# Kernel tuning notes

Hardware: AMD Instinct MI355X
Metric: run time of the kernel (lower is better)

## Reference

```python
import jax, jax.numpy as jnp
import numpy as np
import math

B, T, D = 2, 2048, 2048
H, KV, Dh = 16, 4, 128
REP = H // KV
WINDOW = 1024
META = 128
ROPE_BASE = 10000.0


def _apply_rotary(x, pos):
    # x: (B, h, T, Dh), pos: (T,) -- interleaved (even/odd) RoPE as in the torch module
    dh = x.shape[-1]
    inv = 1.0 / (ROPE_BASE ** (jnp.arange(0, dh, 2, dtype=jnp.float32) / dh))  # (Dh/2,)
    freqs = pos.astype(jnp.float32)[:, None] * inv[None, :]                    # (T, Dh/2)
    cos = jnp.cos(freqs)[None, None].astype(x.dtype)
    sin = jnp.sin(freqs)[None, None].astype(x.dtype)
    x1, x2 = x[..., ::2], x[..., 1::2]
    o1 = x1 * cos - x2 * sin
    o2 = x1 * sin + x2 * cos
    return jnp.stack([o1, o2], axis=-1).reshape(x.shape)


def setup_inputs() -> dict:
    key = jax.random.key(0)
    ks = jax.random.split(key, 5)
    s = 0.02
    return {
        "x": jax.random.normal(ks[0], (B, T, D), jnp.float32),
        "Wq": jax.random.normal(ks[1], (D, H * Dh), jnp.float32) * s,
        "Wk": jax.random.normal(ks[2], (D, KV * Dh), jnp.float32) * s,
        "Wv": jax.random.normal(ks[3], (D, KV * Dh), jnp.float32) * s,
        "Wo": jax.random.normal(ks[4], (H * Dh, D), jnp.float32) * s,
    }


def reference(x, Wq, Wk, Wv, Wo):
    Bx, Tx, _ = x.shape
    # projections + head split: q (B,H,T,Dh); k,v (B,KV,T,Dh)
    q = (x @ Wq).reshape(Bx, Tx, H, Dh).transpose(0, 2, 1, 3)
    k = (x @ Wk).reshape(Bx, Tx, KV, Dh).transpose(0, 2, 1, 3)
    v = (x @ Wv).reshape(Bx, Tx, KV, Dh).transpose(0, 2, 1, 3)
    pos = jnp.arange(Tx)
    q = _apply_rotary(q, pos)
    k = _apply_rotary(k, pos)
    # GQA: repeat kv heads (expand+reshape == contiguous repeat along head axis)
    k_full = jnp.repeat(k, REP, axis=1)
    v_full = jnp.repeat(v, REP, axis=1)
    # sliding window: keep META meta tokens + last w content tokens
    w = min(WINDOW, Tx - META)
    k_full = jnp.concatenate([k_full[:, :, :META], k_full[:, :, Tx - w:]], axis=2)
    v_full = jnp.concatenate([v_full[:, :, :META], v_full[:, :, Tx - w:]], axis=2)
    Tk = META + w
    scores = jnp.einsum("bhqd,bhkd->bhqk", q, k_full) / math.sqrt(Dh)
    # torch: triu(full(-inf,(T,Tk)), diagonal=1) added to scores
    mask = jnp.arange(Tk)[None, :] > jnp.arange(Tx)[:, None]   # (T, Tk)
    scores = jnp.where(mask[None, None], -jnp.inf, scores)
    attn = jax.nn.softmax(scores, axis=-1)
    out = jnp.einsum("bhqk,bhkd->bhqd", attn, v_full)
    out = out.transpose(0, 2, 1, 3).reshape(Bx, Tx, H * Dh)
    return out @ Wo
```

## Files before the change

kernel.cpp:

```cpp
#include <hip/hip_runtime.h>
#include <hip/hip_bf16.h>
#include <math.h>

typedef __attribute__((ext_vector_type(4))) float f32x4;
typedef __attribute__((ext_vector_type(8))) short bf16x8;

#define LDSP(p)  ((__attribute__((address_space(3))) void*)(p))
#define GMEMP(p) ((const __attribute__((address_space(1))) void*)(p))

__device__ __forceinline__ short f2b(float f) {
  __hip_bfloat16 h = __float2bfloat16(f);
  return __builtin_bit_cast(short, h);
}
__device__ __forceinline__ float b2f(short s) {
  __hip_bfloat16 h = __builtin_bit_cast(__hip_bfloat16, s);
  return __bfloat162float(h);
}
__device__ __forceinline__ unsigned pack2(float a, float b) {
  return (unsigned)(unsigned short)f2b(a) | ((unsigned)(unsigned short)f2b(b) << 16);
}

__global__ void cvt_kernel(const float* __restrict__ src, short* __restrict__ dst, int n8) {
  int i = blockIdx.x * blockDim.x + threadIdx.x;
  if (i >= n8) return;
  const float4* s4 = (const float4*)src;
  float4 a = s4[2 * i], b = s4[2 * i + 1];
  bf16x8 o;
  o[0] = f2b(a.x); o[1] = f2b(a.y); o[2] = f2b(a.z); o[3] = f2b(a.w);
  o[4] = f2b(b.x); o[5] = f2b(b.y); o[6] = f2b(b.z); o[7] = f2b(b.w);
  *(bf16x8*)(dst + (size_t)i * 8) = o;
}

__global__ void transpose_kernel(const float* __restrict__ src, short* __restrict__ dst,
                                 int rows, int cols) {
  __shared__ float tile[32][33];
  int c0 = blockIdx.x * 32, r0 = blockIdx.y * 32;
  int tx = threadIdx.x & 31, ty = threadIdx.x >> 5;
  for (int i = ty; i < 32; i += 8)
    tile[i][tx] = src[(size_t)(r0 + i) * cols + c0 + tx];
  __syncthreads();
  for (int i = ty; i < 32; i += 8)
    dst[(size_t)(c0 + i) * rows + r0 + tx] = f2b(tile[tx][i]);
}

template <int OUTBF>
__global__ __launch_bounds__(256) void gemm_bt(const short* __restrict__ A,
                                               const short* __restrict__ Bt,
                                               void* __restrict__ Cv,
                                               int M, int N, int K) {
  __shared__ alignas(16) short As[128 * 32];
  __shared__ alignas(16) short Bs[128 * 32];
  const int m0 = blockIdx.y * 128, n0 = blockIdx.x * 128;
  const int wave = threadIdx.x >> 6, lane = threadIdx.x & 63;
  const int g = lane >> 4, cl = lane & 15;
  const int wr = (wave >> 1) * 64, wc = (wave & 1) * 64;
  f32x4 acc[4][4];
#pragma unroll
  for (int i = 0; i < 4; ++i)
#pragma unroll
    for (int j = 0; j < 4; ++j) acc[i][j] = (f32x4){0.f, 0.f, 0.f, 0.f};

  const size_t lda = (size_t)K;
  for (int kt = 0; kt < K; kt += 32) {
#pragma unroll
    for (int c = 0; c < 2; ++c) {
      int e = (wave * 2 + c) * 512;
      int el = e + lane * 8;
      const short* ga = A + (size_t)(m0 + (el >> 5)) * lda + kt + (el & 31);
      __builtin_amdgcn_global_load_lds(GMEMP(ga), LDSP(&As[e]), 16, 0, 0);
      const short* gb = Bt + (size_t)(n0 + (el >> 5)) * lda + kt + (el & 31);
      __builtin_amdgcn_global_load_lds(GMEMP(gb), LDSP(&Bs[e]), 16, 0, 0);
    }
    __syncthreads();
    bf16x8 af[4], bfr[4];
#pragma unroll
    for (int i = 0; i < 4; ++i)
      af[i] = *(const bf16x8*)&As[(wr + 16 * i + cl) * 32 + 8 * g];
#pragma unroll
    for (int j = 0; j < 4; ++j)
      bfr[j] = *(const bf16x8*)&Bs[(wc + 16 * j + cl) * 32 + 8 * g];
#pragma unroll
    for (int i = 0; i < 4; ++i)
#pragma unroll
      for (int j = 0; j < 4; ++j)
        acc[i][j] = __builtin_amdgcn_mfma_f32_16x16x32_bf16(af[i], bfr[j], acc[i][j], 0, 0, 0);
    __syncthreads();
  }
#pragma unroll
  for (int i = 0; i < 4; ++i)
#pragma unroll
    for (int j = 0; j < 4; ++j)
#pragma unroll
      for (int r = 0; r < 4; ++r) {
        int row = m0 + wr + 16 * i + 4 * g + r;
        int col = n0 + wc + 16 * j + cl;
        if (OUTBF)
          ((short*)Cv)[(size_t)row * N + col] = f2b(acc[i][j][r]);
        else
          ((float*)Cv)[(size_t)row * N + col] = acc[i][j][r];
      }
}

__global__ void rope_q_kernel(const short* __restrict__ qkv, short* __restrict__ qb) {
  int tid = blockIdx.x * 256 + threadIdx.x;
  int i = tid & 63;
  int h = (tid >> 6) & 15;
  int row = tid >> 10;
  int t = row & 2047;
  int b = row >> 11;
  unsigned u = *(const unsigned*)(qkv + (size_t)row * 3072 + h * 128 + 2 * i);
  float x1 = b2f((short)(u & 0xffff));
  float x2 = b2f((short)(u >> 16));
  float inv = exp2f(-0.20762050593046f * (float)i);
  float ang = (float)t * inv;
  float sn, cs;
  __sincosf(ang, &sn, &cs);
  float o1 = x1 * cs - x2 * sn;
  float o2 = x1 * sn + x2 * cs;
  unsigned w = pack2(o1, o2);
  *(unsigned*)(qb + (size_t)((b * 16 + h) * 2048 + t) * 128 + 2 * i) = w;
}

__global__ void rope_k_kernel(const short* __restrict__ qkv, short* __restrict__ ksel) {
  int tid = blockIdx.x * 256 + threadIdx.x;
  int i = tid & 63;
  int kvh = (tid >> 6) & 3;
  int row = tid >> 8;
  int t = row & 2047;
  int b = row >> 11;
  int idx = t < 128 ? t : (t >= 1024 ? t - 896 : -1);
  if (idx < 0) return;
  unsigned u = *(const unsigned*)(qkv + (size_t)row * 3072 + 2048 + kvh * 128 + 2 * i);
  float x1 = b2f((short)(u & 0xffff));
  float x2 = b2f((short)(u >> 16));
  float inv = exp2f(-0.20762050593046f * (float)i);
  float ang = (float)t * inv;
  float sn, cs;
  __sincosf(ang, &sn, &cs);
  float o1 = x1 * cs - x2 * sn;
  float o2 = x1 * sn + x2 * cs;
  unsigned w = pack2(o1, o2);
  *(unsigned*)(ksel + (size_t)((b * 4 + kvh) * 1152 + idx) * 128 + 2 * i) = w;
}

__global__ void vsel_kernel(const short* __restrict__ qkv, short* __restrict__ vt) {
  int tid = blockIdx.x * 256 + threadIdx.x;
  int idx = tid % 1152;
  int rest = tid / 1152;
  int d = rest & 127;
  int kvh = (rest >> 7) & 3;
  int b = rest >> 9;
  int t = idx < 128 ? idx : idx + 896;
  vt[(size_t)((b * 4 + kvh) * 128 + d) * 1152 + idx] =
      qkv[(size_t)(b * 2048 + t) * 3072 + 2560 + kvh * 128 + d];
}

__global__ __launch_bounds__(256) void attn_kernel(const short* __restrict__ qb,
                                                   const short* __restrict__ ksel,
                                                   const short* __restrict__ vt,
                                                   short* __restrict__ ao) {
  __shared__ alignas(16) short Ksm[2][8192];
  __shared__ alignas(16) short Vsm[8192];
  __shared__ alignas(16) short Psm[4][16][72];

  const int blk = blockIdx.x;
  const int qt = 31 - (blk >> 5);
  const int h = blk & 15, b = (blk >> 4) & 1;
  const int kv = h >> 2;
  const int wave = threadIdx.x >> 6, lane = threadIdx.x & 63;
  const int g = lane >> 4, cl = lane & 15;
  const int q0w = qt * 64 + wave * 16;
  const int qi = q0w + cl;
  const float scale = 0.08838834764831845f;
  const int niter = (qt + 1 < 18) ? (qt + 1) : 18;

  const short* kselb = ksel + (size_t)(b * 4 + kv) * 1152 * 128;
  const short* vtb = vt + (size_t)(b * 4 + kv) * 128 * 1152;

  const short* qrow = qb + (size_t)((b * 16 + h) * 2048 + qi) * 128;
  bf16x8 qf[4];
#pragma unroll
  for (int d = 0; d < 4; ++d) qf[d] = *(const bf16x8*)(qrow + d * 32 + 8 * g);

  f32x4 o[8];
#pragma unroll
  for (int c = 0; c < 8; ++c) o[c] = (f32x4){0.f, 0.f, 0.f, 0.f};
  float m_i = -1e30f, l_i = 0.f;

#pragma unroll
  for (int i = 0; i < 4; ++i) {
    int base = i * 2048 + wave * 512;
    int Lel = base + lane * 8;
    int kr = Lel >> 7;
    int kc = (Lel & 127) ^ ((kr & 7) << 3);
    __builtin_amdgcn_global_load_lds(GMEMP(kselb + (size_t)kr * 128 + kc),
                                     LDSP(&Ksm[0][base]), 16, 0, 0);
  }
  asm volatile("s_waitcnt vmcnt(0)" ::: "memory");
  __builtin_amdgcn_s_barrier();
  asm volatile("" ::: "memory");

  int cur = 0;
  for (int t = 0; t < niter; ++t) {
    const int kk0 = t * 64;
#pragma unroll
    for (int i = 0; i < 4; ++i) {
      int base = i * 2048 + wave * 512;
      int Lel = base + lane * 8;
      int vr = Lel >> 6;
      int vc = (Lel & 63) ^ ((vr & 7) << 3);
      __builtin_amdgcn_global_load_lds(GMEMP(vtb + (size_t)vr * 1152 + kk0 + vc),
                                       LDSP(&Vsm[base]), 16, 0, 0);
    }
    const bool lastk = (t + 1 >= niter);
    if (!lastk) {
#pragma unroll
      for (int i = 0; i < 4; ++i) {
        int base = i * 2048 + wave * 512;
        int Lel = base + lane * 8;
        int kr = Lel >> 7;
        int kc = (Lel & 127) ^ ((kr & 7) << 3);
        __builtin_amdgcn_global_load_lds(GMEMP(kselb + (size_t)(kk0 + 64 + kr) * 128 + kc),
                                         LDSP(&Ksm[cur ^ 1][base]), 16, 0, 0);
      }
    }

    f32x4 s[4];
#pragma unroll
    for (int j = 0; j < 4; ++j) s[j] = (f32x4){0.f, 0.f, 0.f, 0.f};
    const short* kb = &Ksm[cur][0];
    const int sw = (cl & 7) << 3;
#pragma unroll
    for (int j = 0; j < 4; ++j) {
      const int rs = (16 * j + cl) * 128;
#pragma unroll
      for (int d = 0; d < 4; ++d) {
        bf16x8 kf = *(const bf16x8*)&kb[rs + ((d * 32 + 8 * g) ^ sw)];
        s[j] = __builtin_amdgcn_mfma_f32_16x16x32_bf16(kf, qf[d], s[j], 0, 0, 0);
      }
    }

    float sv[4][4];
    float mx = -1e30f;
#pragma unroll
    for (int j = 0; j < 4; ++j)
#pragma unroll
      for (int r = 0; r < 4; ++r) {
        int key = kk0 + 16 * j + 4 * g + r;
        float v = s[j][r] * scale;
        v = (key <= qi) ? v : -1e30f;
        sv[j][r] = v;
        mx = fmaxf(mx, v);
      }
    mx = fmaxf(mx, __shfl_xor(mx, 16));
    mx = fmaxf(mx, __shfl_xor(mx, 32));
    const float mnew = fmaxf(m_i, mx);
    const float alpha = __expf(m_i - mnew);
    m_i = mnew;
    float ls = 0.f;
#pragma unroll
    for (int j = 0; j < 4; ++j) {
      float p0 = __expf(sv[j][0] - mnew);
      float p1 = __expf(sv[j][1] - mnew);
      float p2 = __expf(sv[j][2] - mnew);
      float p3 = __expf(sv[j][3] - mnew);
      ls += (p0 + p1) + (p2 + p3);
      uint2 w;
      w.x = pack2(p0, p1);
      w.y = pack2(p2, p3);
      *(uint2*)&Psm[wave][cl][16 * j + 4 * g] = w;
    }
    ls += __shfl_xor(ls, 16);
    ls += __shfl_xor(ls, 32);
    l_i = l_i * alpha + ls;
#pragma unroll
    for (int c = 0; c < 8; ++c)
#pragma unroll
      for (int r = 0; r < 4; ++r) o[c][r] *= alpha;

    if (!lastk)
      asm volatile("s_waitcnt vmcnt(4)" ::: "memory");
    else
      asm volatile("s_waitcnt vmcnt(0)" ::: "memory");
    __builtin_amdgcn_s_barrier();
    asm volatile("" ::: "memory");

    asm volatile("s_waitcnt lgkmcnt(0)" ::: "memory");
    bf16x8 pb0 = *(const bf16x8*)&Psm[wave][cl][8 * g];
    bf16x8 pb1 = *(const bf16x8*)&Psm[wave][cl][32 + 8 * g];
#pragma unroll
    for (int c = 0; c < 8; ++c) {
      const int rowd = c * 16 + cl;
      const int rvs = rowd * 64;
      bf16x8 v0 = *(const bf16x8*)&Vsm[rvs + ((8 * g) ^ sw)];
      bf16x8 v1 = *(const bf16x8*)&Vsm[rvs + ((32 + 8 * g) ^ sw)];
      o[c] = __builtin_amdgcn_mfma_f32_16x16x32_bf16(v0, pb0, o[c], 0, 0, 0);
      o[c] = __builtin_amdgcn_mfma_f32_16x16x32_bf16(v1, pb1, o[c], 0, 0, 0);
    }

    asm volatile("s_waitcnt vmcnt(0)" ::: "memory");
    __builtin_amdgcn_s_barrier();
    asm volatile("" ::: "memory");
    cur ^= 1;
  }

  short* Ol = &Ksm[0][0] + wave * 2176;
  const float invl = 1.0f / l_i;
#pragma unroll
  for (int c = 0; c < 8; ++c) {
    uint2 w;
    w.x = pack2(o[c][0] * invl, o[c][1] * invl);
    w.y = pack2(o[c][2] * invl, o[c][3] * invl);
    *(uint2*)&Ol[cl * 136 + c * 16 + 4 * g] = w;
  }
  asm volatile("s_waitcnt lgkmcnt(0)" ::: "memory");
  const int rowq = lane & 15, seg = lane >> 4;
  const short* srcl = Ol + rowq * 136 + seg * 32;
  short* dst = ao + (size_t)(b * 2048 + q0w + rowq) * 2048 + h * 128 + seg * 32;
#pragma unroll
  for (int k = 0; k < 4; ++k)
    *(bf16x8*)(dst + 8 * k) = *(const bf16x8*)(srcl + 8 * k);
}

extern "C" void kernel_launch(void* const* d_in, const int* in_sizes, int n_in,
                              void* d_out, int out_size, void* d_ws, size_t ws_size,
                              hipStream_t stream) {
  const float* x = (const float*)d_in[0];
  const float* Wq = (const float*)d_in[1];
  const float* Wk = (const float*)d_in[2];
  const float* Wv = (const float*)d_in[3];
  const float* Wo = (const float*)d_in[4];
  float* out = (float*)d_out;

  char* ws = (char*)d_ws;
  short* x_bf = (short*)ws;   ws += (size_t)4096 * 2048 * 2;
  short* wqkv_t = (short*)ws; ws += (size_t)3072 * 2048 * 2;
  short* wo_t = (short*)ws;   ws += (size_t)2048 * 2048 * 2;
  short* qkv = (short*)ws;    ws += (size_t)4096 * 3072 * 2;
  short* q_bf = (short*)ws;   ws += (size_t)2 * 16 * 2048 * 128 * 2;
  short* k_sel = (short*)ws;  ws += (size_t)2 * 4 * 1152 * 128 * 2;
  short* v_t = (short*)ws;    ws += (size_t)2 * 4 * 128 * 1152 * 2;
  short* ao = (short*)ws;     ws += (size_t)4096 * 2048 * 2;

  cvt_kernel<<<4096, 256, 0, stream>>>(x, x_bf, 1048576);
  transpose_kernel<<<dim3(64, 64), 256, 0, stream>>>(Wq, wqkv_t, 2048, 2048);
  transpose_kernel<<<dim3(16, 64), 256, 0, stream>>>(Wk, wqkv_t + (size_t)2048 * 2048, 2048, 512);
  transpose_kernel<<<dim3(16, 64), 256, 0, stream>>>(Wv, wqkv_t + (size_t)2560 * 2048, 2048, 512);
  transpose_kernel<<<dim3(64, 64), 256, 0, stream>>>(Wo, wo_t, 2048, 2048);
  gemm_bt<1><<<dim3(24, 32), 256, 0, stream>>>(x_bf, wqkv_t, qkv, 4096, 3072, 2048);
  rope_q_kernel<<<16384, 256, 0, stream>>>(qkv, q_bf);
  rope_k_kernel<<<4096, 256, 0, stream>>>(qkv, k_sel);
  vsel_kernel<<<4608, 256, 0, stream>>>(qkv, v_t);
  attn_kernel<<<1024, 256, 0, stream>>>(q_bf, k_sel, v_t, ao);
  gemm_bt<0><<<dim3(16, 32), 256, 0, stream>>>(ao, wo_t, out, 4096, 2048, 2048);
}
```

Before: 333.2 us.

## Triple-buffer GEMM with LDS swizzle, double-buffer attention V, merge small launches

The GEMM moves to a three-stage LDS pipeline with an XOR swizzle on its tiles, waits with partial vmcnt barriers, and raises wave priority around the MFMA blocks. The attention kernel double-buffers V as well as K, prefetching both for the next tile and dropping the mid-iteration barrier. The four transpose launches become one kernel, and the three RoPE/select kernels become one, to cut launch overhead. In exchange it uses more LDS per block, which can lower occupancy, and the barrier and vmcnt accounting is harder to get right.

```diff
diff --git a/kernel.cpp b/kernel.cpp
--- a/kernel.cpp
+++ b/kernel.cpp
@@ -31,16 +31,23 @@
   *(bf16x8*)(dst + (size_t)i * 8) = o;
 }
 
-__global__ void transpose_kernel(const float* __restrict__ src, short* __restrict__ dst,
-                                 int rows, int cols) {
+__global__ void transpose_all(const float* __restrict__ Wq, const float* __restrict__ Wk,
+                              const float* __restrict__ Wv, const float* __restrict__ Wo,
+                              short* __restrict__ wqkv_t, short* __restrict__ wo_t) {
   __shared__ float tile[32][33];
-  int c0 = blockIdx.x * 32, r0 = blockIdx.y * 32;
+  int gx = blockIdx.x;
+  const float* src; short* dst; int cols, cx;
+  if (gx < 64)       { src = Wq; dst = wqkv_t;                        cols = 2048; cx = gx; }
+  else if (gx < 80)  { src = Wk; dst = wqkv_t + (size_t)2048 * 2048;  cols = 512;  cx = gx - 64; }
+  else if (gx < 96)  { src = Wv; dst = wqkv_t + (size_t)2560 * 2048;  cols = 512;  cx = gx - 80; }
+  else               { src = Wo; dst = wo_t;                          cols = 2048; cx = gx - 96; }
+  int c0 = cx * 32, r0 = blockIdx.y * 32;
   int tx = threadIdx.x & 31, ty = threadIdx.x >> 5;
   for (int i = ty; i < 32; i += 8)
     tile[i][tx] = src[(size_t)(r0 + i) * cols + c0 + tx];
   __syncthreads();
   for (int i = ty; i < 32; i += 8)
-    dst[(size_t)(c0 + i) * rows + r0 + tx] = f2b(tile[tx][i]);
+    dst[(size_t)(c0 + i) * 2048 + r0 + tx] = f2b(tile[tx][i]);
 }
 
 template <int OUTBF>
@@ -48,44 +55,71 @@
                                                const short* __restrict__ Bt,
                                                void* __restrict__ Cv,
                                                int M, int N, int K) {
-  __shared__ alignas(16) short As[128 * 32];
-  __shared__ alignas(16) short Bs[128 * 32];
+  __shared__ alignas(16) short As[3][128 * 32];
+  __shared__ alignas(16) short Bs[3][128 * 32];
   const int m0 = blockIdx.y * 128, n0 = blockIdx.x * 128;
   const int wave = threadIdx.x >> 6, lane = threadIdx.x & 63;
   const int g = lane >> 4, cl = lane & 15;
   const int wr = (wave >> 1) * 64, wc = (wave & 1) * 64;
+  const int tid = threadIdx.x;
   f32x4 acc[4][4];
 #pragma unroll
   for (int i = 0; i < 4; ++i)
 #pragma unroll
     for (int j = 0; j < 4; ++j) acc[i][j] = (f32x4){0.f, 0.f, 0.f, 0.f};
 
-  const size_t lda = (size_t)K;
-  for (int kt = 0; kt < K; kt += 32) {
-#pragma unroll
-    for (int c = 0; c < 2; ++c) {
-      int e = (wave * 2 + c) * 512;
-      int el = e + lane * 8;
-      const short* ga = A + (size_t)(m0 + (el >> 5)) * lda + kt + (el & 31);
-      __builtin_amdgcn_global_load_lds(GMEMP(ga), LDSP(&As[e]), 16, 0, 0);
-      const short* gb = Bt + (size_t)(n0 + (el >> 5)) * lda + kt + (el & 31);
-      __builtin_amdgcn_global_load_lds(GMEMP(gb), LDSP(&Bs[e]), 16, 0, 0);
-    }
-    __syncthreads();
+  const int e0 = tid * 8;
+#define STAGE(kt, s)                                                                        \
+  {                                                                                         \
+    _Pragma("unroll") for (int c = 0; c < 2; ++c) {                                         \
+      int e = c * 2048 + e0;                                                                \
+      int r = e >> 5;                                                                       \
+      int j = (e >> 3) & 3;                                                                 \
+      int col = (kt) + 8 * (j ^ ((r >> 1) & 3));                                            \
+      __builtin_amdgcn_global_load_lds(GMEMP(A + (size_t)(m0 + r) * K + col),               \
+                                       LDSP(&As[s][e]), 16, 0, 0);                          \
+      __builtin_amdgcn_global_load_lds(GMEMP(Bt + (size_t)(n0 + r) * K + col),              \
+                                       LDSP(&Bs[s][e]), 16, 0, 0);                          \
+    }                                                                                       \
+  }
+
+  const int nkt = K >> 5;
+  STAGE(0, 0);
+  STAGE(32, 1);
+  asm volatile("s_waitcnt vmcnt(4)" ::: "memory");
+  __builtin_amdgcn_s_barrier();
+  asm volatile("" ::: "memory");
+
+  int s = 0;
+  for (int t = 0; t < nkt; ++t) {
+    if (t + 2 < nkt) {
+      int s2 = s + 2; if (s2 >= 3) s2 -= 3;
+      STAGE((t + 2) << 5, s2);
+    }
     bf16x8 af[4], bfr[4];
 #pragma unroll
-    for (int i = 0; i < 4; ++i)
-      af[i] = *(const bf16x8*)&As[(wr + 16 * i + cl) * 32 + 8 * g];
-#pragma unroll
-    for (int j = 0; j < 4; ++j)
-      bfr[j] = *(const bf16x8*)&Bs[(wc + 16 * j + cl) * 32 + 8 * g];
+    for (int i = 0; i < 4; ++i) {
+      int R = wr + 16 * i + cl;
+      af[i] = *(const bf16x8*)&As[s][R * 32 + 8 * (g ^ ((R >> 1) & 3))];
+    }
+#pragma unroll
+    for (int j = 0; j < 4; ++j) {
+      int R = wc + 16 * j + cl;
+      bfr[j] = *(const bf16x8*)&Bs[s][R * 32 + 8 * (g ^ ((R >> 1) & 3))];
+    }
+    __builtin_amdgcn_s_setprio(1);
 #pragma unroll
     for (int i = 0; i < 4; ++i)
 #pragma unroll
       for (int j = 0; j < 4; ++j)
         acc[i][j] = __builtin_amdgcn_mfma_f32_16x16x32_bf16(af[i], bfr[j], acc[i][j], 0, 0, 0);
-    __syncthreads();
-  }
+    __builtin_amdgcn_s_setprio(0);
+    asm volatile("s_waitcnt vmcnt(4)" ::: "memory");
+    __builtin_amdgcn_s_barrier();
+    asm volatile("" ::: "memory");
+    if (++s >= 3) s -= 3;
+  }
+#undef STAGE
 #pragma unroll
   for (int i = 0; i < 4; ++i)
 #pragma unroll
@@ -101,58 +135,54 @@
       }
 }
 
-__global__ void rope_q_kernel(const short* __restrict__ qkv, short* __restrict__ qb) {
-  int tid = blockIdx.x * 256 + threadIdx.x;
-  int i = tid & 63;
-  int h = (tid >> 6) & 15;
-  int row = tid >> 10;
-  int t = row & 2047;
-  int b = row >> 11;
-  unsigned u = *(const unsigned*)(qkv + (size_t)row * 3072 + h * 128 + 2 * i);
-  float x1 = b2f((short)(u & 0xffff));
-  float x2 = b2f((short)(u >> 16));
-  float inv = exp2f(-0.20762050593046f * (float)i);
-  float ang = (float)t * inv;
-  float sn, cs;
-  __sincosf(ang, &sn, &cs);
-  float o1 = x1 * cs - x2 * sn;
-  float o2 = x1 * sn + x2 * cs;
-  unsigned w = pack2(o1, o2);
-  *(unsigned*)(qb + (size_t)((b * 16 + h) * 2048 + t) * 128 + 2 * i) = w;
-}
-
-__global__ void rope_k_kernel(const short* __restrict__ qkv, short* __restrict__ ksel) {
-  int tid = blockIdx.x * 256 + threadIdx.x;
-  int i = tid & 63;
-  int kvh = (tid >> 6) & 3;
-  int row = tid >> 8;
-  int t = row & 2047;
-  int b = row >> 11;
-  int idx = t < 128 ? t : (t >= 1024 ? t - 896 : -1);
-  if (idx < 0) return;
-  unsigned u = *(const unsigned*)(qkv + (size_t)row * 3072 + 2048 + kvh * 128 + 2 * i);
-  float x1 = b2f((short)(u & 0xffff));
-  float x2 = b2f((short)(u >> 16));
-  float inv = exp2f(-0.20762050593046f * (float)i);
-  float ang = (float)t * inv;
-  float sn, cs;
-  __sincosf(ang, &sn, &cs);
-  float o1 = x1 * cs - x2 * sn;
-  float o2 = x1 * sn + x2 * cs;
-  unsigned w = pack2(o1, o2);
-  *(unsigned*)(ksel + (size_t)((b * 4 + kvh) * 1152 + idx) * 128 + 2 * i) = w;
-}
-
-__global__ void vsel_kernel(const short* __restrict__ qkv, short* __restrict__ vt) {
-  int tid = blockIdx.x * 256 + threadIdx.x;
-  int idx = tid % 1152;
-  int rest = tid / 1152;
-  int d = rest & 127;
-  int kvh = (rest >> 7) & 3;
-  int b = rest >> 9;
-  int t = idx < 128 ? idx : idx + 896;
-  vt[(size_t)((b * 4 + kvh) * 128 + d) * 1152 + idx] =
-      qkv[(size_t)(b * 2048 + t) * 3072 + 2560 + kvh * 128 + d];
+__global__ void pp_kernel(const short* __restrict__ qkv, short* __restrict__ qb,
+                          short* __restrict__ ksel, short* __restrict__ vt) {
+  int blk = blockIdx.x;
+  if (blk < 16384) {
+    int tid = blk * 256 + threadIdx.x;
+    int i = tid & 63;
+    int h = (tid >> 6) & 15;
+    int row = tid >> 10;
+    int t = row & 2047;
+    int b = row >> 11;
+    unsigned u = *(const unsigned*)(qkv + (size_t)row * 3072 + h * 128 + 2 * i);
+    float x1 = b2f((short)(u & 0xffff));
+    float x2 = b2f((short)(u >> 16));
+    float inv = exp2f(-0.20762050593046f * (float)i);
+    float ang = (float)t * inv;
+    float sn, cs;
+    __sincosf(ang, &sn, &cs);
+    unsigned w = pack2(x1 * cs - x2 * sn, x1 * sn + x2 * cs);
+    *(unsigned*)(qb + (size_t)((b * 16 + h) * 2048 + t) * 128 + 2 * i) = w;
+  } else if (blk < 16384 + 4096) {
+    int tid = (blk - 16384) * 256 + threadIdx.x;
+    int i = tid & 63;
+    int kvh = (tid >> 6) & 3;
+    int row = tid >> 8;
+    int t = row & 2047;
+    int b = row >> 11;
+    int idx = t < 128 ? t : (t >= 1024 ? t - 896 : -1);
+    if (idx < 0) return;
+    unsigned u = *(const unsigned*)(qkv + (size_t)row * 3072 + 2048 + kvh * 128 + 2 * i);
+    float x1 = b2f((short)(u & 0xffff));
+    float x2 = b2f((short)(u >> 16));
+    float inv = exp2f(-0.20762050593046f * (float)i);
+    float ang = (float)t * inv;
+    float sn, cs;
+    __sincosf(ang, &sn, &cs);
+    unsigned w = pack2(x1 * cs - x2 * sn, x1 * sn + x2 * cs);
+    *(unsigned*)(ksel + (size_t)((b * 4 + kvh) * 1152 + idx) * 128 + 2 * i) = w;
+  } else {
+    int tid = (blk - 20480) * 256 + threadIdx.x;
+    int idx = tid % 1152;
+    int rest = tid / 1152;
+    int d = rest & 127;
+    int kvh = (rest >> 7) & 3;
+    int b = rest >> 9;
+    int t = idx < 128 ? idx : idx + 896;
+    vt[(size_t)((b * 4 + kvh) * 128 + d) * 1152 + idx] =
+        qkv[(size_t)(b * 2048 + t) * 3072 + 2560 + kvh * 128 + d];
+  }
 }
 
 __global__ __launch_bounds__(256) void attn_kernel(const short* __restrict__ qb,
@@ -160,7 +190,7 @@
                                                    const short* __restrict__ vt,
                                                    short* __restrict__ ao) {
   __shared__ alignas(16) short Ksm[2][8192];
-  __shared__ alignas(16) short Vsm[8192];
+  __shared__ alignas(16) short Vsm[2][8192];
   __shared__ alignas(16) short Psm[4][16][72];
 
   const int blk = blockIdx.x;
@@ -187,58 +217,59 @@
   for (int c = 0; c < 8; ++c) o[c] = (f32x4){0.f, 0.f, 0.f, 0.f};
   float m_i = -1e30f, l_i = 0.f;
 
-#pragma unroll
-  for (int i = 0; i < 4; ++i) {
-    int base = i * 2048 + wave * 512;
-    int Lel = base + lane * 8;
-    int kr = Lel >> 7;
-    int kc = (Lel & 127) ^ ((kr & 7) << 3);
-    __builtin_amdgcn_global_load_lds(GMEMP(kselb + (size_t)kr * 128 + kc),
-                                     LDSP(&Ksm[0][base]), 16, 0, 0);
-  }
+#define STAGEK(kk0, buf)                                                                  \
+  {                                                                                       \
+    _Pragma("unroll") for (int i = 0; i < 4; ++i) {                                       \
+      int base = i * 2048 + wave * 512;                                                   \
+      int Lel = base + lane * 8;                                                          \
+      int kr = Lel >> 7;                                                                  \
+      int kc = (Lel & 127) ^ ((kr & 7) << 3);                                             \
+      __builtin_amdgcn_global_load_lds(GMEMP(kselb + (size_t)((kk0) + kr) * 128 + kc),    \
+                                       LDSP(&Ksm[buf][base]), 16, 0, 0);                  \
+    }                                                                                     \
+  }
+#define STAGEV(kk0, buf)                                                                  \
+  {                                                                                       \
+    _Pragma("unroll") for (int i = 0; i < 4; ++i) {                                       \
+      int base = i * 2048 + wave * 512;                                                   \
+      int Lel = base + lane * 8;                                                          \
+      int vr = Lel >> 6;                                                                  \
+      int vc = (Lel & 63) ^ ((vr & 7) << 3);                                              \
+      __builtin_amdgcn_global_load_lds(GMEMP(vtb + (size_t)vr * 1152 + (kk0) + vc),       \
+                                       LDSP(&Vsm[buf][base]), 16, 0, 0);                  \
+    }                                                                                     \
+  }
+
+  STAGEK(0, 0);
+  STAGEV(0, 0);
   asm volatile("s_waitcnt vmcnt(0)" ::: "memory");
   __builtin_amdgcn_s_barrier();
   asm volatile("" ::: "memory");
 
-  int cur = 0;
   for (int t = 0; t < niter; ++t) {
+    const int cur = t & 1;
     const int kk0 = t * 64;
-#pragma unroll
-    for (int i = 0; i < 4; ++i) {
-      int base = i * 2048 + wave * 512;
-      int Lel = base + lane * 8;
-      int vr = Lel >> 6;
-      int vc = (Lel & 63) ^ ((vr & 7) << 3);
-      __builtin_amdgcn_global_load_lds(GMEMP(vtb + (size_t)vr * 1152 + kk0 + vc),
-                                       LDSP(&Vsm[base]), 16, 0, 0);
-    }
-    const bool lastk = (t + 1 >= niter);
-    if (!lastk) {
-#pragma unroll
-      for (int i = 0; i < 4; ++i) {
-        int base = i * 2048 + wave * 512;
-        int Lel = base + lane * 8;
-        int kr = Lel >> 7;
-        int kc = (Lel & 127) ^ ((kr & 7) << 3);
-        __builtin_amdgcn_global_load_lds(GMEMP(kselb + (size_t)(kk0 + 64 + kr) * 128 + kc),
-                                         LDSP(&Ksm[cur ^ 1][base]), 16, 0, 0);
-      }
-    }
-
-    f32x4 s[4];
-#pragma unroll
-    for (int j = 0; j < 4; ++j) s[j] = (f32x4){0.f, 0.f, 0.f, 0.f};
+    if (t + 1 < niter) {
+      STAGEK(kk0 + 64, cur ^ 1);
+      STAGEV(kk0 + 64, cur ^ 1);
+    }
+
+    f32x4 sf[4];
+#pragma unroll
+    for (int j = 0; j < 4; ++j) sf[j] = (f32x4){0.f, 0.f, 0.f, 0.f};
     const short* kb = &Ksm[cur][0];
     const int sw = (cl & 7) << 3;
+    __builtin_amdgcn_s_setprio(1);
 #pragma unroll
     for (int j = 0; j < 4; ++j) {
       const int rs = (16 * j + cl) * 128;
 #pragma unroll
       for (int d = 0; d < 4; ++d) {
         bf16x8 kf = *(const bf16x8*)&kb[rs + ((d * 32 + 8 * g) ^ sw)];
-        s[j] = __builtin_amdgcn_mfma_f32_16x16x32_bf16(kf, qf[d], s[j], 0, 0, 0);
+        sf[j] = __builtin_amdgcn_mfma_f32_16x16x32_bf16(kf, qf[d], sf[j], 0, 0, 0);
       }
     }
+    __builtin_amdgcn_s_setprio(0);
 
     float sv[4][4];
     float mx = -1e30f;
@@ -247,7 +278,7 @@
 #pragma unroll
       for (int r = 0; r < 4; ++r) {
         int key = kk0 + 16 * j + 4 * g + r;
-        float v = s[j][r] * scale;
+        float v = sf[j][r] * scale;
         v = (key <= qi) ? v : -1e30f;
         sv[j][r] = v;
         mx = fmaxf(mx, v);
@@ -278,31 +309,27 @@
 #pragma unroll
       for (int r = 0; r < 4; ++r) o[c][r] *= alpha;
 
-    if (!lastk)
-      asm volatile("s_waitcnt vmcnt(4)" ::: "memory");
-    else
-      asm volatile("s_waitcnt vmcnt(0)" ::: "memory");
-    __builtin_amdgcn_s_barrier();
-    asm volatile("" ::: "memory");
-
     asm volatile("s_waitcnt lgkmcnt(0)" ::: "memory");
     bf16x8 pb0 = *(const bf16x8*)&Psm[wave][cl][8 * g];
     bf16x8 pb1 = *(const bf16x8*)&Psm[wave][cl][32 + 8 * g];
+    const short* vb = &Vsm[cur][0];
+    __builtin_amdgcn_s_setprio(1);
 #pragma unroll
     for (int c = 0; c < 8; ++c) {
-      const int rowd = c * 16 + cl;
-      const int rvs = rowd * 64;
-      bf16x8 v0 = *(const bf16x8*)&Vsm[rvs + ((8 * g) ^ sw)];
-      bf16x8 v1 = *(const bf16x8*)&Vsm[rvs + ((32 + 8 * g) ^ sw)];
+      const int rvs = (c * 16 + cl) * 64;
+      bf16x8 v0 = *(const bf16x8*)&vb[rvs + ((8 * g) ^ sw)];
+      bf16x8 v1 = *(const bf16x8*)&vb[rvs + ((32 + 8 * g) ^ sw)];
       o[c] = __builtin_amdgcn_mfma_f32_16x16x32_bf16(v0, pb0, o[c], 0, 0, 0);
       o[c] = __builtin_amdgcn_mfma_f32_16x16x32_bf16(v1, pb1, o[c], 0, 0, 0);
     }
+    __builtin_amdgcn_s_setprio(0);
 
     asm volatile("s_waitcnt vmcnt(0)" ::: "memory");
     __builtin_amdgcn_s_barrier();
     asm volatile("" ::: "memory");
-    cur ^= 1;
-  }
+  }
+#undef STAGEK
+#undef STAGEV
 
   short* Ol = &Ksm[0][0] + wave * 2176;
   const float invl = 1.0f / l_i;
@@ -343,14 +370,9 @@
   short* ao = (short*)ws;     ws += (size_t)4096 * 2048 * 2;
 
   cvt_kernel<<<4096, 256, 0, stream>>>(x, x_bf, 1048576);
-  transpose_kernel<<<dim3(64, 64), 256, 0, stream>>>(Wq, wqkv_t, 2048, 2048);
-  transpose_kernel<<<dim3(16, 64), 256, 0, stream>>>(Wk, wqkv_t + (size_t)2048 * 2048, 2048, 512);
-  transpose_kernel<<<dim3(16, 64), 256, 0, stream>>>(Wv, wqkv_t + (size_t)2560 * 2048, 2048, 512);
-  transpose_kernel<<<dim3(64, 64), 256, 0, stream>>>(Wo, wo_t, 2048, 2048);
+  transpose_all<<<dim3(160, 64), 256, 0, stream>>>(Wq, Wk, Wv, Wo, wqkv_t, wo_t);
   gemm_bt<1><<<dim3(24, 32), 256, 0, stream>>>(x_bf, wqkv_t, qkv, 4096, 3072, 2048);
-  rope_q_kernel<<<16384, 256, 0, stream>>>(qkv, q_bf);
-  rope_k_kernel<<<4096, 256, 0, stream>>>(qkv, k_sel);
-  vsel_kernel<<<4608, 256, 0, stream>>>(qkv, v_t);
+  pp_kernel<<<25088, 256, 0, stream>>>(qkv, q_bf, k_sel, v_t);
   attn_kernel<<<1024, 256, 0, stream>>>(q_bf, k_sel, v_t, ao);
   gemm_bt<0><<<dim3(16, 32), 256, 0, stream>>>(ao, wo_t, out, 4096, 2048, 2048);
 }
```

After: 321.0 us. 1.04x faster.
